# Optimization experiments

Hardware: AMD Instinct MI355X
Metric: run time of the kernel (lower is better)

## Reference

```python
import jax, jax.numpy as jnp
import numpy as np

# Standard SMPL kinematic tree parents (kintree_table)
PARENTS = np.array([-1, 0, 0, 0, 1, 2, 3, 4, 5, 6, 7, 8, 9, 9, 9,
                    12, 13, 14, 16, 17, 18, 19, 20, 21])
NV, NJ, NB, NP = 6890, 24, 10, 207


def rodrigues(r):
    """Axis-angle [N,3] -> rotation matrices [N,3,3] (Rodrigues formula)."""
    theta = jnp.linalg.norm(r, axis=1, keepdims=True) + 1e-8  # [N,1]
    rh = r / theta                                            # [N,3]
    cos = jnp.cos(theta)[..., None]                           # [N,1,1]
    sin = jnp.sin(theta)[..., None]
    z = jnp.zeros_like(rh[:, 0])
    m = jnp.stack([z, -rh[:, 2], rh[:, 1],
                   rh[:, 2], z, -rh[:, 0],
                   -rh[:, 1], rh[:, 0], z], axis=1).reshape(-1, 3, 3)
    dot = rh[:, :, None] * rh[:, None, :]                     # outer product
    eye = jnp.eye(3, dtype=r.dtype)
    return cos * eye + (1.0 - cos) * dot + sin * m


def setup_inputs() -> dict:
    key = jax.random.key(0)
    ks = jax.random.split(key, 9)
    B = 512
    betas = jax.random.normal(ks[0], (B, NB), dtype=jnp.float32)
    thetas = jax.random.normal(ks[1], (B, NJ * 3), dtype=jnp.float32) * 0.3
    trans = jax.random.normal(ks[2], (B, 3), dtype=jnp.float32)
    scale = jnp.ones((1,), dtype=jnp.float32)
    v_template = jax.random.normal(ks[3], (NV, 3), dtype=jnp.float32)
    shapedirs = jax.random.normal(ks[4], (NV, 3, NB), dtype=jnp.float32) * 0.01
    posedirs = jax.random.normal(ks[5], (NV, 3, NP), dtype=jnp.float32) * 0.01
    Jr = jax.random.uniform(ks[6], (NJ, NV), dtype=jnp.float32)
    J_regressor = Jr / jnp.sum(Jr, axis=1, keepdims=True)
    w = jax.random.uniform(ks[7], (NV, NJ), dtype=jnp.float32)
    weights = w / jnp.sum(w, axis=1, keepdims=True)
    return {"betas": betas, "thetas": thetas, "trans": trans, "scale": scale,
            "v_template": v_template, "shapedirs": shapedirs,
            "posedirs": posedirs, "J_regressor": J_regressor,
            "weights": weights}


def reference(betas, thetas, trans, scale, v_template, shapedirs, posedirs,
              J_regressor, weights):
    B = betas.shape[0]
    dt = betas.dtype
    # Shape blend shapes: v_shaped [B, 6890, 3]
    v_shaped = jnp.einsum('bs,vcs->bvc', betas, shapedirs) + v_template
    # Rest-pose joints J(beta): [B, 24, 3]
    J = jnp.einsum('jv,bvc->bjc', J_regressor, v_shaped)
    # Local rotations from axis-angle, root scaled by `scale`
    lRs = rodrigues(thetas.reshape(-1, 3)).reshape(B, NJ, 3, 3)
    lRs = lRs.at[:, 0].multiply(scale[0])
    # Local joint offsets: root keeps J[:,0], children use J[i] - J[parent[i]]
    parents = jnp.asarray(PARENTS)
    t = J - J[:, jnp.clip(parents, 0)]
    t = t.at[:, 0].set(J[:, 0])
    # Local 4x4 transforms [B, 24, 4, 4]
    top = jnp.concatenate([lRs, t[..., None]], axis=3)          # [B,24,3,4]
    bottom = jnp.broadcast_to(jnp.array([0., 0., 0., 1.], dtype=dt),
                              (B, NJ, 1, 4))
    A = jnp.concatenate([top, bottom], axis=2)
    # Kinematic chain accumulation (fixed 24-joint tree)
    results = [A[:, 0]]
    for i in range(1, NJ):
        results.append(results[PARENTS[i]] @ A[:, i])
    stacked = jnp.stack(results, axis=1)                         # [B,24,4,4]
    # Remove rest-pose joint locations from translation column
    Jh = jnp.concatenate([J, jnp.zeros((B, NJ, 1), dtype=dt)], axis=2)
    deformed = jnp.einsum('bjxy,bjy->bjx', stacked, Jh)          # [B,24,4]
    G = stacked.at[..., 3].add(-deformed)
    # Pose blend shapes from non-root rotations
    lrotmin = (lRs[:, 1:] - jnp.eye(3, dtype=dt)).reshape(B, -1)  # [B,207]
    v_posed = v_shaped + jnp.einsum('bp,vcp->bvc', lrotmin, posedirs)
    # Linear blend skinning
    T = jnp.einsum('bjxy,vj->bvxy', G, weights)                  # [B,6890,4,4]
    vh = jnp.concatenate([v_posed, jnp.ones((B, NV, 1), dtype=dt)], axis=2)
    v = jnp.einsum('bvxy,bvy->bvx', T, vh)[:, :, :3]
    result = v + trans[:, None, :]
    joints = jnp.einsum('jv,bvc->bjc', J_regressor, result)
    return result, joints
```

## Files before the change

kernel.cpp:

```cpp
#include <hip/hip_runtime.h>

#define NVERT 6890
#define NJNT  24
#define NBETA 10
#define NPOSE 207
#define NBATCH 512
#define KPAD 224
#define MROWS 20736
#define NVC (NVERT * 3)

#define NBA 18144
#define NBW 1728
#define NJR 576

typedef __attribute__((ext_vector_type(8))) short short8;
typedef __attribute__((ext_vector_type(4))) float floatx4;

__constant__ int c_par[NJNT]   = {-1,0,0,0,1,2,3,4,5,6,7,8,9,9,9,12,13,14,16,17,18,19,20,21};
__constant__ int c_depth[NJNT] = { 0,1,1,1,2,2,2,3,3,3,4,4,4,4,4,5,5,5,6,6,7,7,8,8};

static __device__ __forceinline__ unsigned short f2bf(float x) {
  union { float f; unsigned u; } v; v.f = x;
  unsigned r = (v.u + 0x7FFFu + ((v.u >> 16) & 1u)) >> 16;
  return (unsigned short)r;
}
static __device__ __forceinline__ float bf2f(unsigned short h) {
  union { unsigned u; float f; } v; v.u = (unsigned)h << 16;
  return v.f;
}

typedef __attribute__((address_space(1))) const void as1_void;
typedef __attribute__((address_space(3))) void as3_void;
static __device__ __forceinline__ void gl_lds16(const void* g, void* l) {
  __builtin_amdgcn_global_load_lds((as1_void*)g, (as3_void*)l, 16, 0, 0);
}

__global__ __launch_bounds__(256) void k_prep(
    const float* __restrict__ pdir, const float* __restrict__ sd,
    const float* __restrict__ vt, const float* __restrict__ wgt,
    const float* __restrict__ Jr,
    unsigned short* __restrict__ AT, unsigned short* __restrict__ W16,
    float* __restrict__ wsJP) {
  const int bx = blockIdx.x;
  const int tid = threadIdx.x;
  if (bx < NBA) {
    const int idx = bx * 256 + tid;
    const int kk = idx & 31;
    const int row = (idx >> 5) % MROWS;
    const int kt = idx / (MROWS * 32);
    const int k = kt * 32 + kk;
    float val = 0.f;
    if (row < NVC) {
      if (k < NPOSE)            val = pdir[(size_t)row * NPOSE + k];
      else if (k < NPOSE + 10)  val = sd[(size_t)row * 10 + (k - NPOSE)];
      else if (k == NPOSE + 10) val = vt[row];
    }
    AT[idx] = f2bf(val);
  } else if (bx < NBA + NBW) {
    const int idx = (bx - NBA) * 256 + tid;
    const int v = idx >> 6, c = idx & 63, j = c & 31;
    const float w = (v < NVERT && j < 24) ? wgt[(size_t)v * 24 + j] : 0.f;
    const unsigned short hi = f2bf(w);
    W16[idx] = (c >> 5) ? f2bf(w - bf2f(hi)) : hi;
  } else {
    const int jb = bx - (NBA + NBW);
    const int jc = jb % 72, j = jc / 3, c = jc % 3;
    const int chunk = jb / 72;
    const int v0 = chunk * 864;
    const int vend = min(NVERT, v0 + 864);
    float acc[11];
    #pragma unroll
    for (int k = 0; k < 11; ++k) acc[k] = 0.f;
    for (int v = v0 + tid; v < vend; v += 256) {
      const float w = Jr[j * NVERT + v];
      acc[0] += w * vt[v * 3 + c];
      const float* s = sd + (size_t)v * 30 + c * 10;
      #pragma unroll
      for (int k = 0; k < 10; ++k) acc[1 + k] += w * s[k];
    }
    #pragma unroll
    for (int off = 32; off > 0; off >>= 1) {
      #pragma unroll
      for (int k = 0; k < 11; ++k) acc[k] += __shfl_down(acc[k], off, 64);
    }
    __shared__ float red[4][11];
    const int lane = tid & 63, wv = tid >> 6;
    if (lane == 0) {
      #pragma unroll
      for (int k = 0; k < 11; ++k) red[wv][k] = acc[k];
    }
    __syncthreads();
    if (tid == 0) {
      #pragma unroll
      for (int k = 0; k < 11; ++k)
        wsJP[(size_t)(chunk * 72 + jc) * 11 + k] =
            red[0][k] + red[1][k] + red[2][k] + red[3][k];
    }
  }
}

__global__ __launch_bounds__(256, 2) void k_chain3(
    const float* __restrict__ betas, const float* __restrict__ thetas,
    const float* __restrict__ scale, const float* __restrict__ trans,
    const float* __restrict__ wsJP,
    unsigned short* __restrict__ BT, unsigned short* __restrict__ G16,
    float* __restrict__ jzero) {
  __shared__ __align__(16) float sJ[792];
  __shared__ __align__(16) float sJJ[4][72];
  __shared__ __align__(16) float sM[4][288];
  __shared__ __align__(16) unsigned short sG[4][1024];
  __shared__ __align__(16) unsigned short sB[4][KPAD];

  const int tid = threadIdx.x;
  const int wv = tid >> 6, lane = tid & 63;
  const int b = blockIdx.x * 4 + wv;

  for (int z = blockIdx.x * 256 + tid; z < NBATCH * 72; z += 32768)
    jzero[z] = 0.f;

  if (tid < 72) {
    #pragma unroll
    for (int k = 0; k < 11; ++k) {
      float s = 0.f;
      #pragma unroll
      for (int c8 = 0; c8 < 8; ++c8) s += wsJP[(size_t)(c8 * 72 + tid) * 11 + k];
      if (k == 0) sJ[tid] = s;
      else        sJ[72 + tid * 10 + (k - 1)] = s;
    }
  }
  #pragma unroll
  for (int r = 0; r < 4; ++r) {
    sG[wv][lane * 16 + r * 4 + 0] = 0; sG[wv][lane * 16 + r * 4 + 1] = 0;
    sG[wv][lane * 16 + r * 4 + 2] = 0; sG[wv][lane * 16 + r * 4 + 3] = 0;
  }
  __syncthreads();

  float R[9], t[3], M[12], Jx = 0.f, Jy = 0.f, Jz = 0.f;
  const int i = lane;
  if (i < NJNT) {
    #pragma unroll
    for (int c = 0; c < 3; ++c) {
      float a = sJ[i * 3 + c];
      const float* d = sJ + 72 + (i * 3 + c) * 10;
      #pragma unroll
      for (int s = 0; s < NBETA; ++s) a += d[s] * betas[b * NBETA + s];
      if (c == 0) Jx = a; else if (c == 1) Jy = a; else Jz = a;
    }
    sJJ[wv][i * 3 + 0] = Jx; sJJ[wv][i * 3 + 1] = Jy; sJJ[wv][i * 3 + 2] = Jz;
    const float rx = thetas[b * 72 + i * 3 + 0];
    const float ry = thetas[b * 72 + i * 3 + 1];
    const float rz = thetas[b * 72 + i * 3 + 2];
    const float th = sqrtf(rx * rx + ry * ry + rz * rz) + 1e-8f;
    const float inv = 1.f / th;
    const float x = rx * inv, y = ry * inv, z = rz * inv;
    const float cs = cosf(th), sn = sinf(th), omc = 1.f - cs;
    R[0] = cs + omc * x * x;     R[1] = omc * x * y - sn * z; R[2] = omc * x * z + sn * y;
    R[3] = omc * x * y + sn * z; R[4] = cs + omc * y * y;     R[5] = omc * y * z - sn * x;
    R[6] = omc * x * z - sn * y; R[7] = omc * y * z + sn * x; R[8] = cs + omc * z * z;
    if (i == 0) {
      const float sc = scale[0];
      #pragma unroll
      for (int k = 0; k < 9; ++k) R[k] *= sc;
    } else {
      #pragma unroll
      for (int k = 0; k < 9; ++k)
        sB[wv][(i - 1) * 9 + k] = f2bf(R[k] - ((k == 0 || k == 4 || k == 8) ? 1.f : 0.f));
    }
  }
  if (i == 0) {
    #pragma unroll
    for (int s = 0; s < NBETA; ++s) sB[wv][NPOSE + s] = f2bf(betas[b * NBETA + s]);
    sB[wv][NPOSE + 10] = 0x3F80;
    #pragma unroll
    for (int k = NPOSE + 11; k < KPAD; ++k) sB[wv][k] = 0;
  }
  __syncthreads();

  if (i < NJNT) {
    if (i == 0) { t[0] = Jx; t[1] = Jy; t[2] = Jz; }
    else {
      const int p = c_par[i];
      t[0] = Jx - sJJ[wv][p * 3 + 0];
      t[1] = Jy - sJJ[wv][p * 3 + 1];
      t[2] = Jz - sJJ[wv][p * 3 + 2];
    }
    if (i == 0) {
      #pragma unroll
      for (int r = 0; r < 3; ++r) {
        M[r*4+0] = R[r*3+0]; M[r*4+1] = R[r*3+1]; M[r*4+2] = R[r*3+2]; M[r*4+3] = t[r];
      }
      #pragma unroll
      for (int k = 0; k < 12; ++k) sM[wv][k] = M[k];
    }
  }
  __syncthreads();

  for (int lvl = 1; lvl <= 8; ++lvl) {
    if (i < NJNT && c_depth[i] == lvl) {
      const float* Mp = sM[wv] + c_par[i] * 12;
      #pragma unroll
      for (int r = 0; r < 3; ++r) {
        const float p0 = Mp[r*4+0], p1 = Mp[r*4+1], p2 = Mp[r*4+2], p3 = Mp[r*4+3];
        M[r*4+0] = p0*R[0] + p1*R[3] + p2*R[6];
        M[r*4+1] = p0*R[1] + p1*R[4] + p2*R[7];
        M[r*4+2] = p0*R[2] + p1*R[5] + p2*R[8];
        M[r*4+3] = p0*t[0] + p1*t[1] + p2*t[2] + p3;
      }
      #pragma unroll
      for (int k = 0; k < 12; ++k) sM[wv][i * 12 + k] = M[k];
    }
    __syncthreads();
  }

  if (i < NJNT) {
    #pragma unroll
    for (int r = 0; r < 3; ++r) {
      M[r*4+3] = M[r*4+3] - (M[r*4+0]*Jx + M[r*4+1]*Jy + M[r*4+2]*Jz)
               + trans[b * 3 + r];
    }
    #pragma unroll
    for (int e = 0; e < 12; ++e) {
      const float g = M[e];
      const unsigned short hi = f2bf(g);
      sG[wv][e * 32 + i]       = hi;
      sG[wv][512 + e * 32 + i] = f2bf(g - bf2f(hi));
    }
  }
  __syncthreads();

  *(uint4*)(G16 + (size_t)b * 1024 + lane * 16)     = *(uint4*)&sG[wv][lane * 16];
  *(uint4*)(G16 + (size_t)b * 1024 + lane * 16 + 8) = *(uint4*)&sG[wv][lane * 16 + 8];
  if (lane < 28)
    *(uint4*)(BT + ((size_t)(lane >> 2) * NBATCH + b) * 32 + (lane & 3) * 8) =
        *(uint4*)&sB[wv][lane * 8];
}

__global__ __launch_bounds__(256, 4) void k_skin4(
    const unsigned short* __restrict__ AT, const unsigned short* __restrict__ BT,
    const unsigned short* __restrict__ W16, const unsigned short* __restrict__ G16,
    float* __restrict__ out) {
  __shared__ __align__(16) char smem[33536];
  float* sV           = (float*)smem;
  unsigned short* sG2 = (unsigned short*)(smem + 13056);

  const int tid = threadIdx.x;
  const int wv = tid >> 6, lane = tid & 63;
  const int q = lane >> 4, n = lane & 15;

  const int fb = blockIdx.x;
  const int vb = (fb & 7) * 216 + (fb >> 3);
  const int b0 = (vb & 15) * 32;
  const int by = vb >> 4;
  const int vc0 = by * 192;

  floatx4 acc[3][2];
  #pragma unroll
  for (int mt = 0; mt < 3; ++mt)
    #pragma unroll
    for (int nt = 0; nt < 2; ++nt) acc[mt][nt] = (floatx4)(0.f);

  const int stoff = (lane >> 2) * 32 + (((lane & 3) ^ ((lane >> 3) & 3)) * 8);
  const int rslot = ((lane >> 4) ^ ((lane >> 1) & 3)) * 8;

  const unsigned short* gA0 = AT + ((size_t)vc0 + 48 * wv) * 32 + stoff;
  const unsigned short* gB0 = BT + ((size_t)b0 + 16 * wv) * 32 + stoff;

  {
    unsigned short* la = (unsigned short*)smem + 48 * wv * 32;
    gl_lds16(gA0,        la);
    gl_lds16(gA0 + 512,  la + 512);
    gl_lds16(gA0 + 1024, la + 1024);
    if (wv < 2) {
      unsigned short* lb = (unsigned short*)(smem + 12288) + 16 * wv * 32;
      gl_lds16(gB0, lb);
    }
  }
  __syncthreads();

  int cur = 0;
  for (int kt = 0; kt < 7; ++kt) {
    if (kt < 6) {
      const int nb = (cur ^ 1) * 14336;
      unsigned short* la = (unsigned short*)(smem + nb) + 48 * wv * 32;
      const unsigned short* ga = gA0 + (size_t)(kt + 1) * MROWS * 32;
      gl_lds16(ga,        la);
      gl_lds16(ga + 512,  la + 512);
      gl_lds16(ga + 1024, la + 1024);
      if (wv < 2) {
        unsigned short* lb = (unsigned short*)(smem + nb + 12288) + 16 * wv * 32;
        gl_lds16(gB0 + (size_t)(kt + 1) * NBATCH * 32, lb);
      }
    }
    const unsigned short* sAc = (const unsigned short*)(smem + cur * 14336);
    const unsigned short* sBc = sAc + 6144;
    short8 af[3], bfr[2];
    #pragma unroll
    for (int mt = 0; mt < 3; ++mt)
      af[mt] = *(const short8*)(sAc + (48 * wv + 16 * mt + n) * 32 + rslot);
    #pragma unroll
    for (int nt = 0; nt < 2; ++nt)
      bfr[nt] = *(const short8*)(sBc + (16 * nt + n) * 32 + rslot);
    #pragma unroll
    for (int mt = 0; mt < 3; ++mt)
      #pragma unroll
      for (int nt = 0; nt < 2; ++nt)
        acc[mt][nt] = __builtin_amdgcn_mfma_f32_16x16x32_bf16(
            af[mt], bfr[nt], acc[mt][nt], 0, 0, 0);
    __syncthreads();
    cur ^= 1;
  }

  short8 wh[4], wl[4];
  #pragma unroll
  for (int vt = 0; vt < 4; ++vt) {
    const unsigned short* wr = W16 + (size_t)(by * 64 + vt * 16 + n) * 64;
    wh[vt] = *(const short8*)(wr + q * 8);
    wl[vt] = *(const short8*)(wr + 32 + q * 8);
  }

  for (int nt = 0; nt < 2; ++nt) {
    for (int s = 0; s < 2; ++s) {
      __syncthreads();
      if (s == 0) {
        #pragma unroll
        for (int mt = 0; mt < 3; ++mt)
          #pragma unroll
          for (int r = 0; r < 4; ++r)
            sV[(48 * wv + 16 * mt + 4 * q + r) * 17 + n] = acc[mt][nt][r];
      }
      const int bg0 = b0 + nt * 16 + s * 8;
      for (int i = tid; i < 1024; i += 256) {
        const int row = i >> 2, c4 = i & 3;
        const int t = row >> 5, rem = row & 31;
        *(uint4*)(sG2 + row * 40 + c4 * 8) =
            *(const uint4*)(G16 + (size_t)(bg0 + t) * 1024 + rem * 32 + c4 * 8);
      }
      __syncthreads();
      #pragma unroll
      for (int bb = 0; bb < 2; ++bb) {
        const int t = wv * 2 + bb;
        const int col = s * 8 + t;
        const int bg = b0 + nt * 16 + col;
        const short8 gh = *(const short8*)(sG2 + (t * 32 + n) * 40 + q * 8);
        const short8 gl = *(const short8*)(sG2 + (t * 32 + 16 + n) * 40 + q * 8);
        #pragma unroll
        for (int vt = 0; vt < 4; ++vt) {
          floatx4 a2 = (floatx4)(0.f);
          a2 = __builtin_amdgcn_mfma_f32_16x16x32_bf16(gh, wl[vt], a2, 0, 0, 0);
          a2 = __builtin_amdgcn_mfma_f32_16x16x32_bf16(gl, wh[vt], a2, 0, 0, 0);
          a2 = __builtin_amdgcn_mfma_f32_16x16x32_bf16(gh, wh[vt], a2, 0, 0, 0);
          const float X = sV[(48 * vt + 3 * n + 0) * 17 + col];
          const float Y = sV[(48 * vt + 3 * n + 1) * 17 + col];
          const float Z = sV[(48 * vt + 3 * n + 2) * 17 + col];
          const float o = a2[0] * X + a2[1] * Y + a2[2] * Z + a2[3];
          const int vc = vc0 + 48 * vt + 3 * n + q;
          if (q < 3 && vc < NVC)
            out[(size_t)bg * NVC + vc] = o;
        }
      }
    }
  }
}

__global__ __launch_bounds__(256) void k_jnt1(
    const float* __restrict__ Jr, const float* __restrict__ res,
    float* __restrict__ joints) {
  const int b0 = blockIdx.x * 2;
  const int chunk = blockIdx.y;
  const int v0 = chunk * 864;
  const int vend = min(NVERT, v0 + 864);
  const int lane = threadIdx.x & 63, wv = threadIdx.x >> 6;
  float acc[36];
  #pragma unroll
  for (int k = 0; k < 36; ++k) acc[k] = 0.f;
  const float* rA = res + (size_t)b0 * NVC;
  const float* rB = res + (size_t)(b0 + 1) * NVC;
  for (int v = v0 + lane; v < vend; v += 64) {
    const float a0 = rA[v * 3 + 0], a1 = rA[v * 3 + 1], a2 = rA[v * 3 + 2];
    const float e0 = rB[v * 3 + 0], e1 = rB[v * 3 + 1], e2 = rB[v * 3 + 2];
    #pragma unroll
    for (int k = 0; k < 6; ++k) {
      const int j = wv + 4 * k;
      const float w = Jr[j * NVERT + v];
      acc[k*6+0] += w * a0; acc[k*6+1] += w * a1; acc[k*6+2] += w * a2;
      acc[k*6+3] += w * e0; acc[k*6+4] += w * e1; acc[k*6+5] += w * e2;
    }
  }
  #pragma unroll
  for (int off = 32; off > 0; off >>= 1) {
    #pragma unroll
    for (int k = 0; k < 36; ++k) acc[k] += __shfl_down(acc[k], off, 64);
  }
  if (lane == 0) {
    #pragma unroll
    for (int k = 0; k < 6; ++k) {
      const int j = wv + 4 * k;
      atomicAdd(&joints[(size_t)b0 * 72 + j * 3 + 0], acc[k*6+0]);
      atomicAdd(&joints[(size_t)b0 * 72 + j * 3 + 1], acc[k*6+1]);
      atomicAdd(&joints[(size_t)b0 * 72 + j * 3 + 2], acc[k*6+2]);
      atomicAdd(&joints[(size_t)(b0 + 1) * 72 + j * 3 + 0], acc[k*6+3]);
      atomicAdd(&joints[(size_t)(b0 + 1) * 72 + j * 3 + 1], acc[k*6+4]);
      atomicAdd(&joints[(size_t)(b0 + 1) * 72 + j * 3 + 2], acc[k*6+5]);
    }
  }
}

extern "C" void kernel_launch(void* const* d_in, const int* in_sizes, int n_in,
                              void* d_out, int out_size, void* d_ws, size_t ws_size,
                              hipStream_t stream) {
  const float* betas  = (const float*)d_in[0];
  const float* thetas = (const float*)d_in[1];
  const float* trans  = (const float*)d_in[2];
  const float* scale  = (const float*)d_in[3];
  const float* vtpl   = (const float*)d_in[4];
  const float* sd     = (const float*)d_in[5];
  const float* pdir   = (const float*)d_in[6];
  const float* Jr     = (const float*)d_in[7];
  const float* wgt    = (const float*)d_in[8];
  float* out = (float*)d_out;
  float* joints = out + (size_t)NBATCH * NVC;

  float* ws   = (float*)d_ws;
  float* wsJP = ws;
  unsigned short* AT  = (unsigned short*)(ws + 6336);
  unsigned short* BT  = AT + (size_t)MROWS * KPAD;
  unsigned short* W16 = BT + (size_t)NBATCH * KPAD;
  unsigned short* G16 = W16 + (size_t)6912 * 64;

  k_prep<<<NBA + NBW + NJR, 256, 0, stream>>>(pdir, sd, vtpl, wgt, Jr, AT, W16, wsJP);
  k_chain3<<<NBATCH / 4, 256, 0, stream>>>(betas, thetas, scale, trans, wsJP, BT, G16, joints);
  k_skin4<<<1728, 256, 0, stream>>>(AT, BT, W16, G16, out);
  k_jnt1<<<dim3(NBATCH / 2, 8), 256, 0, stream>>>(Jr, out, joints);
}
```

Baseline: 180.6 us.

## Widen skinning GEMM tile to 64 batches and replace async LDS loads with padded copies

```diff
diff --git a/kernel.cpp b/kernel.cpp
--- a/kernel.cpp
+++ b/kernel.cpp
@@ -27,12 +27,6 @@
 static __device__ __forceinline__ float bf2f(unsigned short h) {
   union { unsigned u; float f; } v; v.u = (unsigned)h << 16;
   return v.f;
-}
-
-typedef __attribute__((address_space(1))) const void as1_void;
-typedef __attribute__((address_space(3))) void as3_void;
-static __device__ __forceinline__ void gl_lds16(const void* g, void* l) {
-  __builtin_amdgcn_global_load_lds((as1_void*)g, (as3_void*)l, 16, 0, 0);
 }
 
 __global__ __launch_bounds__(256) void k_prep(
@@ -235,11 +229,13 @@
         *(uint4*)&sB[wv][lane * 8];
 }
 
-__global__ __launch_bounds__(256, 4) void k_skin4(
+__global__ __launch_bounds__(256, 3) void k_skin4(
     const unsigned short* __restrict__ AT, const unsigned short* __restrict__ BT,
     const unsigned short* __restrict__ W16, const unsigned short* __restrict__ G16,
     float* __restrict__ out) {
   __shared__ __align__(16) char smem[33536];
+  unsigned short* sAs = (unsigned short*)smem;
+  unsigned short* sBs = (unsigned short*)(smem + 15360);
   float* sV           = (float*)smem;
   unsigned short* sG2 = (unsigned short*)(smem + 13056);
 
@@ -248,66 +244,41 @@
   const int q = lane >> 4, n = lane & 15;
 
   const int fb = blockIdx.x;
-  const int vb = (fb & 7) * 216 + (fb >> 3);
-  const int b0 = (vb & 15) * 32;
-  const int by = vb >> 4;
+  const int vb = (fb & 7) * 108 + (fb >> 3);
+  const int b0 = (vb & 7) * 64;
+  const int by = vb >> 3;
   const int vc0 = by * 192;
 
-  floatx4 acc[3][2];
+  floatx4 acc[3][4];
   #pragma unroll
   for (int mt = 0; mt < 3; ++mt)
     #pragma unroll
-    for (int nt = 0; nt < 2; ++nt) acc[mt][nt] = (floatx4)(0.f);
-
-  const int stoff = (lane >> 2) * 32 + (((lane & 3) ^ ((lane >> 3) & 3)) * 8);
-  const int rslot = ((lane >> 4) ^ ((lane >> 1) & 3)) * 8;
-
-  const unsigned short* gA0 = AT + ((size_t)vc0 + 48 * wv) * 32 + stoff;
-  const unsigned short* gB0 = BT + ((size_t)b0 + 16 * wv) * 32 + stoff;
-
-  {
-    unsigned short* la = (unsigned short*)smem + 48 * wv * 32;
-    gl_lds16(gA0,        la);
-    gl_lds16(gA0 + 512,  la + 512);
-    gl_lds16(gA0 + 1024, la + 1024);
-    if (wv < 2) {
-      unsigned short* lb = (unsigned short*)(smem + 12288) + 16 * wv * 32;
-      gl_lds16(gB0, lb);
-    }
-  }
-  __syncthreads();
-
-  int cur = 0;
+    for (int nt = 0; nt < 4; ++nt) acc[mt][nt] = (floatx4)(0.f);
+
+  const int srow = tid >> 2, sj = tid & 3;
+
   for (int kt = 0; kt < 7; ++kt) {
-    if (kt < 6) {
-      const int nb = (cur ^ 1) * 14336;
-      unsigned short* la = (unsigned short*)(smem + nb) + 48 * wv * 32;
-      const unsigned short* ga = gA0 + (size_t)(kt + 1) * MROWS * 32;
-      gl_lds16(ga,        la);
-      gl_lds16(ga + 512,  la + 512);
-      gl_lds16(ga + 1024, la + 1024);
-      if (wv < 2) {
-        unsigned short* lb = (unsigned short*)(smem + nb + 12288) + 16 * wv * 32;
-        gl_lds16(gB0 + (size_t)(kt + 1) * NBATCH * 32, lb);
-      }
-    }
-    const unsigned short* sAc = (const unsigned short*)(smem + cur * 14336);
-    const unsigned short* sBc = sAc + 6144;
-    short8 af[3], bfr[2];
+    if (kt) __syncthreads();
+    #pragma unroll
+    for (int it = 0; it < 3; ++it)
+      *(uint4*)(sAs + (it * 64 + srow) * 40 + sj * 8) =
+          *(const uint4*)(AT + ((size_t)kt * MROWS + vc0 + it * 64 + srow) * 32 + sj * 8);
+    *(uint4*)(sBs + srow * 40 + sj * 8) =
+        *(const uint4*)(BT + ((size_t)kt * NBATCH + b0 + srow) * 32 + sj * 8);
+    __syncthreads();
+    short8 af[3], bfr[4];
     #pragma unroll
     for (int mt = 0; mt < 3; ++mt)
-      af[mt] = *(const short8*)(sAc + (48 * wv + 16 * mt + n) * 32 + rslot);
-    #pragma unroll
-    for (int nt = 0; nt < 2; ++nt)
-      bfr[nt] = *(const short8*)(sBc + (16 * nt + n) * 32 + rslot);
+      af[mt] = *(const short8*)(sAs + (48 * wv + 16 * mt + n) * 40 + q * 8);
+    #pragma unroll
+    for (int nt = 0; nt < 4; ++nt)
+      bfr[nt] = *(const short8*)(sBs + (16 * nt + n) * 40 + q * 8);
     #pragma unroll
     for (int mt = 0; mt < 3; ++mt)
       #pragma unroll
-      for (int nt = 0; nt < 2; ++nt)
+      for (int nt = 0; nt < 4; ++nt)
         acc[mt][nt] = __builtin_amdgcn_mfma_f32_16x16x32_bf16(
             af[mt], bfr[nt], acc[mt][nt], 0, 0, 0);
-    __syncthreads();
-    cur ^= 1;
   }
 
   short8 wh[4], wl[4];
@@ -318,7 +289,7 @@
     wl[vt] = *(const short8*)(wr + 32 + q * 8);
   }
 
-  for (int nt = 0; nt < 2; ++nt) {
+  for (int nt = 0; nt < 4; ++nt) {
     for (int s = 0; s < 2; ++s) {
       __syncthreads();
       if (s == 0) {
@@ -429,6 +400,6 @@
 
   k_prep<<<NBA + NBW + NJR, 256, 0, stream>>>(pdir, sd, vtpl, wgt, Jr, AT, W16, wsJP);
   k_chain3<<<NBATCH / 4, 256, 0, stream>>>(betas, thetas, scale, trans, wsJP, BT, G16, joints);
-  k_skin4<<<1728, 256, 0, stream>>>(AT, BT, W16, G16, out);
+  k_skin4<<<864, 256, 0, stream>>>(AT, BT, W16, G16, out);
   k_jnt1<<<dim3(NBATCH / 2, 8), 256, 0, stream>>>(Jr, out, joints);
 }
```

Result: faster. 176.9 us (-2.1%).
